# Optimization experiments

Hardware: AMD Instinct MI355X
Metric: run time of the kernel (lower is better)

The kernel has to match this reference:

```python
import jax, jax.numpy as jnp
import numpy as np

B, N, C, H, W = 16, 64, 128, 64, 64
IMG = 512.0
SCALE = 0.125          # spatial_scale
MAX_GRID = 16          # >= ceil(max_roi_side * SCALE); boxes built so sides <= 128px -> 16
OUT_CH = 256


def setup_inputs() -> dict:
    key = jax.random.key(0)
    k1, k2, k3, k4, k5 = jax.random.split(key, 5)
    z = jax.random.normal(k1, (B, C, H, W), jnp.float32)
    xy = jax.random.uniform(k2, (B, N, 2), jnp.float32, 0.0, IMG - 128.0)
    wh = jax.random.uniform(k3, (B, N, 2), jnp.float32, 8.0, 128.0)
    bboxes = jnp.concatenate([xy, xy + wh], axis=-1)  # [B,N,4] xyxy, image coords
    W_out = jax.random.normal(k4, (OUT_CH, C), jnp.float32) / np.sqrt(C).astype(np.float32)
    b_out = jax.random.normal(k5, (OUT_CH,), jnp.float32) * 0.01
    return {"z": z, "bboxes": bboxes, "W_out": W_out, "b_out": b_out}


def _prep_coord(c, L):
    # torchvision bilinear edge handling; c: sample coord, L: spatial extent
    inr = (c > -1.0) & (c < float(L))          # out of range -> value 0 (still counted)
    cc = jnp.clip(c, 0.0, None)
    lo = jnp.minimum(jnp.floor(cc).astype(jnp.int32), L - 1)
    hi = jnp.minimum(lo + 1, L - 1)
    cc = jnp.where(lo >= L - 1, lo.astype(c.dtype), cc)
    frac = cc - lo.astype(c.dtype)
    return lo, hi, frac, inr


def roi_align_1x1(z, boxes, scale=SCALE, max_grid=MAX_GRID):
    # z: [B,C,H,W], boxes: [B,N,4] xyxy. torchvision roi_align, output_size=1,
    # aligned=True, sampling_ratio=-1 (adaptive grid = ceil(roi_side), masked to max_grid).
    Bz, Cz, Hh, Ww = z.shape
    b = boxes * scale - 0.5                       # aligned=True offset
    x1, y1, x2, y2 = b[..., 0], b[..., 1], b[..., 2], b[..., 3]
    roi_w, roi_h = x2 - x1, y2 - y1               # [B,N]
    gw = jnp.clip(jnp.ceil(roi_w), 1.0, float(max_grid))
    gh = jnp.clip(jnp.ceil(roi_h), 1.0, float(max_grid))
    g = jnp.arange(max_grid, dtype=z.dtype)
    sy = y1[..., None] + (g + 0.5) * (roi_h / gh)[..., None]   # [B,N,G]
    sx = x1[..., None] + (g + 0.5) * (roi_w / gw)[..., None]
    vy = g < gh[..., None]                        # grid-validity (adaptive count)
    vx = g < gw[..., None]

    yl, yh, fy, iry = _prep_coord(sy, Hh)
    xl, xh, fx, irx = _prep_coord(sx, Ww)
    hy, hx = 1.0 - fy, 1.0 - fx

    zf = z.transpose(0, 2, 3, 1)                  # [B,H,W,C]
    shp = (Bz, boxes.shape[1], max_grid, max_grid)
    Yl = jnp.broadcast_to(yl[..., :, None], shp)
    Yh = jnp.broadcast_to(yh[..., :, None], shp)
    Xl = jnp.broadcast_to(xl[..., None, :], shp)
    Xh = jnp.broadcast_to(xh[..., None, :], shp)

    gather = jax.vmap(lambda zb, yi, xi: zb[yi, xi])   # -> [B,N,G,G,C]
    v11 = gather(zf, Yl, Xl)
    v12 = gather(zf, Yl, Xh)
    v21 = gather(zf, Yh, Xl)
    v22 = gather(zf, Yh, Xh)

    w11 = hy[..., :, None] * hx[..., None, :]
    w12 = hy[..., :, None] * fx[..., None, :]
    w21 = fy[..., :, None] * hx[..., None, :]
    w22 = fy[..., :, None] * fx[..., None, :]
    val = (w11[..., None] * v11 + w12[..., None] * v12
           + w21[..., None] * v21 + w22[..., None] * v22)   # [B,N,G,G,C]

    mask = ((vy[..., :, None] & vx[..., None, :])
            & (iry[..., :, None] & irx[..., None, :])).astype(z.dtype)
    val = val * mask[..., None]
    count = (gh * gw)[..., None]                   # adaptive sample count
    return val.sum(axis=(2, 3)) / count            # [B,N,C]


def reference(z, bboxes, W_out, b_out):
    # roi_align (output 1x1) -> avgpool(1) is identity -> reshape [B,N,C] -> Linear
    feats = roi_align_1x1(z, bboxes)               # [B,N,C]
    return feats @ W_out.T + b_out                 # [B,N,OUT_CH]
```

## Files before the change

kernel.cpp:

```cpp
#include <hip/hip_runtime.h>

#define B_ 16
#define N_ 64
#define C_ 128
#define H_ 64
#define W_ 64
#define HW_ (H_ * W_)
#define OUT_CH_ 256
#define MAX_GRID_ 16
#define SCALE_ 0.125f

__device__ __forceinline__ unsigned short f2bf(float f) {
  unsigned int u = __float_as_uint(f);
  u = (u + 0x7fffu + ((u >> 16) & 1u)) >> 16;
  return (unsigned short)u;
}

__global__ __launch_bounds__(256) void transpose_bf16_kernel(
    const float* __restrict__ z, unsigned short* __restrict__ zf) {
  __shared__ unsigned short tile[128 * 129];
  const int b  = blockIdx.y;
  const int pt = blockIdx.x;
  const int t  = threadIdx.x;

  const float* zb = z + (size_t)b * C_ * HW_;
#pragma unroll
  for (int iter = 0; iter < 16; ++iter) {
    int idx = iter * 256 + t;
    int c   = idx >> 5;
    int p4  = (idx & 31) << 2;
    float4 v = *(const float4*)(zb + (size_t)c * HW_ + pt * 128 + p4);
    tile[(p4 + 0) * 129 + c] = f2bf(v.x);
    tile[(p4 + 1) * 129 + c] = f2bf(v.y);
    tile[(p4 + 2) * 129 + c] = f2bf(v.z);
    tile[(p4 + 3) * 129 + c] = f2bf(v.w);
  }
  __syncthreads();

  unsigned short* zfb = zf + (size_t)b * HW_ * C_;
#pragma unroll
  for (int iter = 0; iter < 8; ++iter) {
    int idx = iter * 256 + t;
    int p   = idx >> 4;
    int k8  = (idx & 15) << 3;
    const unsigned short* src = &tile[p * 129 + k8];
    uint4 u;
    u.x = (unsigned int)src[0] | ((unsigned int)src[1] << 16);
    u.y = (unsigned int)src[2] | ((unsigned int)src[3] << 16);
    u.z = (unsigned int)src[4] | ((unsigned int)src[5] << 16);
    u.w = (unsigned int)src[6] | ((unsigned int)src[7] << 16);
    *(uint4*)(zfb + (size_t)(pt * 128 + p) * C_ + k8) = u;
  }
}

__global__ __launch_bounds__(256) void wtrans_kernel(
    const float* __restrict__ Wm, float* __restrict__ Wt) {
  __shared__ float tile[32][33];
  int ot = blockIdx.x;
  int ct = blockIdx.y;
  int j = threadIdx.x, i0 = threadIdx.y;
#pragma unroll
  for (int k = 0; k < 4; ++k) {
    int i = i0 + k * 8;
    tile[i][j] = Wm[(size_t)(ot * 32 + i) * C_ + ct * 32 + j];
  }
  __syncthreads();
#pragma unroll
  for (int k = 0; k < 4; ++k) {
    int i = i0 + k * 8;
    Wt[(size_t)(ct * 32 + i) * OUT_CH_ + ot * 32 + j] = tile[j][i];
  }
}

__global__ __launch_bounds__(128) void gather_kernel(
    const unsigned short* __restrict__ zf,
    const float* __restrict__ boxes,
    float* __restrict__ partial)
{
  int bid = blockIdx.x;
  int roi = bid >> 3;
  int t   = threadIdx.x;
  int gy  = ((bid & 7) << 1) + (t >> 6);
  int c2  = t & 63;

  float4 bx = ((const float4*)boxes)[roi];
  float x1 = bx.x * SCALE_ - 0.5f;
  float y1 = bx.y * SCALE_ - 0.5f;
  float roi_w = bx.z * SCALE_ - 0.5f - x1;
  float roi_h = bx.w * SCALE_ - 0.5f - y1;
  float gwf = fminf(fmaxf(ceilf(roi_w), 1.0f), (float)MAX_GRID_);
  float ghf = fminf(fmaxf(ceilf(roi_h), 1.0f), (float)MAX_GRID_);
  int gw = (int)gwf;
  int gh = (int)ghf;
  if (gy >= gh) return;

  float stepx = roi_w / gwf;
  float stepy = roi_h / ghf;

  float sy = y1 + ((float)gy + 0.5f) * stepy;
  bool iry = (sy > -1.0f) && (sy < (float)H_);
  float acc0 = 0.0f, acc1 = 0.0f;

  if (iry) {
    float cy = fmaxf(sy, 0.0f);
    int yl = (int)cy;
    yl = yl < (H_ - 1) ? yl : (H_ - 1);
    int yh = (yl + 1) < (H_ - 1) ? (yl + 1) : (H_ - 1);
    if (yl >= H_ - 1) cy = (float)yl;
    float fy = cy - (float)yl;
    float hy = 1.0f - fy;

    const unsigned short* zb = zf + (size_t)(roi >> 6) * (HW_ * C_);
    const unsigned short* rowl = zb + (size_t)yl * W_ * C_;
    const unsigned short* rowh = zb + (size_t)yh * W_ * C_;
    int co = c2 << 1;

    for (int gx = 0; gx < gw; ++gx) {
      float sx = x1 + ((float)gx + 0.5f) * stepx;
      bool irx = (sx > -1.0f) && (sx < (float)W_);
      if (!irx) continue;
      float cx = fmaxf(sx, 0.0f);
      int xl = (int)cx;
      xl = xl < (W_ - 1) ? xl : (W_ - 1);
      int xh = (xl + 1) < (W_ - 1) ? (xl + 1) : (W_ - 1);
      if (xl >= W_ - 1) cx = (float)xl;
      float fx = cx - (float)xl;
      float hx = 1.0f - fx;

      float w11 = hy * hx, w12 = hy * fx, w21 = fy * hx, w22 = fy * fx;
      unsigned int v11 = *(const unsigned int*)(rowl + xl * C_ + co);
      unsigned int v12 = *(const unsigned int*)(rowl + xh * C_ + co);
      unsigned int v21 = *(const unsigned int*)(rowh + xl * C_ + co);
      unsigned int v22 = *(const unsigned int*)(rowh + xh * C_ + co);

      acc0 += w11 * __uint_as_float(v11 << 16)
            + w12 * __uint_as_float(v12 << 16)
            + w21 * __uint_as_float(v21 << 16)
            + w22 * __uint_as_float(v22 << 16);
      acc1 += w11 * __uint_as_float(v11 & 0xffff0000u)
            + w12 * __uint_as_float(v12 & 0xffff0000u)
            + w21 * __uint_as_float(v21 & 0xffff0000u)
            + w22 * __uint_as_float(v22 & 0xffff0000u);
    }
  }

  float2 res = make_float2(acc0, acc1);
  *(float2*)(partial + (size_t)(roi * MAX_GRID_ + gy) * C_ + (c2 << 1)) = res;
}

__global__ __launch_bounds__(256) void final_kernel(
    const float* __restrict__ partial,
    const float* __restrict__ boxes,
    const float* __restrict__ Wt,
    const float* __restrict__ bias,
    float* __restrict__ out)
{
  int roi = blockIdx.x;
  int t   = threadIdx.x;
  int c   = t & 127;
  int h   = t >> 7;

  float4 bx = ((const float4*)boxes)[roi];
  float roi_w = (bx.z - bx.x) * SCALE_;
  float roi_h = (bx.w - bx.y) * SCALE_;
  float gwf = fminf(fmaxf(ceilf(roi_w), 1.0f), (float)MAX_GRID_);
  float ghf = fminf(fmaxf(ceilf(roi_h), 1.0f), (float)MAX_GRID_);
  int gh = (int)ghf;

  float s = 0.0f;
  for (int gy = h; gy < gh; gy += 2)
    s += partial[(size_t)(roi * MAX_GRID_ + gy) * C_ + c];

  __shared__ float tmp[256];
  __shared__ float feat[128];
  tmp[t] = s;
  __syncthreads();
  if (t < 128) feat[t] = (tmp[t] + tmp[t + 128]) * (1.0f / (ghf * gwf));
  __syncthreads();

  float sum = bias[t];
#pragma unroll
  for (int k = 0; k < C_; k += 4) {
    float4 f = *(const float4*)&feat[k];
    sum += f.x * Wt[(size_t)(k + 0) * OUT_CH_ + t]
         + f.y * Wt[(size_t)(k + 1) * OUT_CH_ + t]
         + f.z * Wt[(size_t)(k + 2) * OUT_CH_ + t]
         + f.w * Wt[(size_t)(k + 3) * OUT_CH_ + t];
  }
  out[(size_t)roi * OUT_CH_ + t] = sum;
}

extern "C" void kernel_launch(void* const* d_in, const int* in_sizes, int n_in,
                              void* d_out, int out_size, void* d_ws, size_t ws_size,
                              hipStream_t stream) {
  const float* z     = (const float*)d_in[0];
  const float* boxes = (const float*)d_in[1];
  const float* Wm    = (const float*)d_in[2];
  const float* bias  = (const float*)d_in[3];
  float* out = (float*)d_out;

  char* ws = (char*)d_ws;
  unsigned short* zf = (unsigned short*)ws;
  float* partial = (float*)(ws + (size_t)B_ * HW_ * C_ * 2);
  float* Wt = (float*)(ws + (size_t)B_ * HW_ * C_ * 2
                          + (size_t)B_ * N_ * MAX_GRID_ * C_ * 4);

  transpose_bf16_kernel<<<dim3(HW_ / 128, B_), 256, 0, stream>>>(z, zf);
  wtrans_kernel<<<dim3(OUT_CH_ / 32, C_ / 32), dim3(32, 8), 0, stream>>>(Wm, Wt);
  gather_kernel<<<B_ * N_ * (MAX_GRID_ / 2), 128, 0, stream>>>(zf, boxes, partial);
  final_kernel<<<B_ * N_, 256, 0, stream>>>(partial, boxes, Wt, bias, out);
}
```

Measured before the change: 107.9 us.

## Fuse ROI gather and linear projection into one kernel per ROI

```diff
diff --git a/kernel.cpp b/kernel.cpp
--- a/kernel.cpp
+++ b/kernel.cpp
@@ -72,16 +72,18 @@
   }
 }
 
-__global__ __launch_bounds__(128) void gather_kernel(
+__global__ __launch_bounds__(256) void roi_fused_kernel(
     const unsigned short* __restrict__ zf,
     const float* __restrict__ boxes,
-    float* __restrict__ partial)
+    const float* __restrict__ Wt,
+    const float* __restrict__ bias,
+    float* __restrict__ out)
 {
-  int bid = blockIdx.x;
-  int roi = bid >> 3;
+  int roi = blockIdx.x;
   int t   = threadIdx.x;
-  int gy  = ((bid & 7) << 1) + (t >> 6);
+  int wv  = t >> 6;
   int c2  = t & 63;
+  int co  = c2 << 1;
 
   float4 bx = ((const float4*)boxes)[roi];
   float x1 = bx.x * SCALE_ - 0.5f;
@@ -92,16 +94,15 @@
   float ghf = fminf(fmaxf(ceilf(roi_h), 1.0f), (float)MAX_GRID_);
   int gw = (int)gwf;
   int gh = (int)ghf;
-  if (gy >= gh) return;
-
   float stepx = roi_w / gwf;
   float stepy = roi_h / ghf;
 
-  float sy = y1 + ((float)gy + 0.5f) * stepy;
-  bool iry = (sy > -1.0f) && (sy < (float)H_);
+  const unsigned short* zb = zf + (size_t)(roi >> 6) * (HW_ * C_);
+
   float acc0 = 0.0f, acc1 = 0.0f;
-
-  if (iry) {
+  for (int gy = wv; gy < gh; gy += 4) {
+    float sy = y1 + ((float)gy + 0.5f) * stepy;
+    float wy = (sy > -1.0f && sy < (float)H_) ? 1.0f : 0.0f;
     float cy = fmaxf(sy, 0.0f);
     int yl = (int)cy;
     yl = yl < (H_ - 1) ? yl : (H_ - 1);
@@ -109,16 +110,12 @@
     if (yl >= H_ - 1) cy = (float)yl;
     float fy = cy - (float)yl;
     float hy = 1.0f - fy;
-
-    const unsigned short* zb = zf + (size_t)(roi >> 6) * (HW_ * C_);
     const unsigned short* rowl = zb + (size_t)yl * W_ * C_;
     const unsigned short* rowh = zb + (size_t)yh * W_ * C_;
-    int co = c2 << 1;
 
     for (int gx = 0; gx < gw; ++gx) {
       float sx = x1 + ((float)gx + 0.5f) * stepx;
-      bool irx = (sx > -1.0f) && (sx < (float)W_);
-      if (!irx) continue;
+      float wx = (sx > -1.0f && sx < (float)W_) ? 1.0f : 0.0f;
       float cx = fmaxf(sx, 0.0f);
       int xl = (int)cx;
       xl = xl < (W_ - 1) ? xl : (W_ - 1);
@@ -127,7 +124,9 @@
       float fx = cx - (float)xl;
       float hx = 1.0f - fx;
 
-      float w11 = hy * hx, w12 = hy * fx, w21 = fy * hx, w22 = fy * fx;
+      float m   = wy * wx;
+      float w11 = hy * hx * m, w12 = hy * fx * m;
+      float w21 = fy * hx * m, w22 = fy * fx * m;
       unsigned int v11 = *(const unsigned int*)(rowl + xl * C_ + co);
       unsigned int v12 = *(const unsigned int*)(rowl + xh * C_ + co);
       unsigned int v21 = *(const unsigned int*)(rowh + xl * C_ + co);
@@ -144,50 +143,26 @@
     }
   }
 
-  float2 res = make_float2(acc0, acc1);
-  *(float2*)(partial + (size_t)(roi * MAX_GRID_ + gy) * C_ + (c2 << 1)) = res;
-}
-
-__global__ __launch_bounds__(256) void final_kernel(
-    const float* __restrict__ partial,
-    const float* __restrict__ boxes,
-    const float* __restrict__ Wt,
-    const float* __restrict__ bias,
-    float* __restrict__ out)
-{
-  int roi = blockIdx.x;
-  int t   = threadIdx.x;
-  int c   = t & 127;
-  int h   = t >> 7;
-
-  float4 bx = ((const float4*)boxes)[roi];
-  float roi_w = (bx.z - bx.x) * SCALE_;
-  float roi_h = (bx.w - bx.y) * SCALE_;
-  float gwf = fminf(fmaxf(ceilf(roi_w), 1.0f), (float)MAX_GRID_);
-  float ghf = fminf(fmaxf(ceilf(roi_h), 1.0f), (float)MAX_GRID_);
-  int gh = (int)ghf;
-
-  float s = 0.0f;
-  for (int gy = h; gy < gh; gy += 2)
-    s += partial[(size_t)(roi * MAX_GRID_ + gy) * C_ + c];
-
-  __shared__ float tmp[256];
+  __shared__ float red[4][128];
   __shared__ float feat[128];
-  tmp[t] = s;
+  red[wv][co]     = acc0;
+  red[wv][co + 1] = acc1;
   __syncthreads();
-  if (t < 128) feat[t] = (tmp[t] + tmp[t + 128]) * (1.0f / (ghf * gwf));
+  if (t < 128) {
+    feat[t] = (red[0][t] + red[1][t] + red[2][t] + red[3][t])
+              * (1.0f / (ghf * gwf));
+  }
   __syncthreads();
 
-  float sum = bias[t];
-#pragma unroll
+  float s0 = bias[t], s1 = 0.0f, s2 = 0.0f, s3 = 0.0f;
+#pragma unroll 4
   for (int k = 0; k < C_; k += 4) {
-    float4 f = *(const float4*)&feat[k];
-    sum += f.x * Wt[(size_t)(k + 0) * OUT_CH_ + t]
-         + f.y * Wt[(size_t)(k + 1) * OUT_CH_ + t]
-         + f.z * Wt[(size_t)(k + 2) * OUT_CH_ + t]
-         + f.w * Wt[(size_t)(k + 3) * OUT_CH_ + t];
+    s0 += feat[k + 0] * Wt[(size_t)(k + 0) * OUT_CH_ + t];
+    s1 += feat[k + 1] * Wt[(size_t)(k + 1) * OUT_CH_ + t];
+    s2 += feat[k + 2] * Wt[(size_t)(k + 2) * OUT_CH_ + t];
+    s3 += feat[k + 3] * Wt[(size_t)(k + 3) * OUT_CH_ + t];
   }
-  out[(size_t)roi * OUT_CH_ + t] = sum;
+  out[(size_t)roi * OUT_CH_ + t] = (s0 + s1) + (s2 + s3);
 }
 
 extern "C" void kernel_launch(void* const* d_in, const int* in_sizes, int n_in,
@@ -201,12 +176,9 @@
 
   char* ws = (char*)d_ws;
   unsigned short* zf = (unsigned short*)ws;
-  float* partial = (float*)(ws + (size_t)B_ * HW_ * C_ * 2);
-  float* Wt = (float*)(ws + (size_t)B_ * HW_ * C_ * 2
-                          + (size_t)B_ * N_ * MAX_GRID_ * C_ * 4);
+  float* Wt = (float*)(ws + (size_t)B_ * HW_ * C_ * 2);
 
   transpose_bf16_kernel<<<dim3(HW_ / 128, B_), 256, 0, stream>>>(z, zf);
   wtrans_kernel<<<dim3(OUT_CH_ / 32, C_ / 32), dim3(32, 8), 0, stream>>>(Wm, Wt);
-  gather_kernel<<<B_ * N_ * (MAX_GRID_ / 2), 128, 0, stream>>>(zf, boxes, partial);
-  final_kernel<<<B_ * N_, 256, 0, stream>>>(partial, boxes, Wt, bias, out);
+  roi_fused_kernel<<<B_ * N_, 256, 0, stream>>>(zf, boxes, Wt, bias, out);
 }
```

After: 112.1 us. +3.9%, slower.
